# Performance work log

Hardware: AMD Instinct MI355X
Metric: run time of the kernel (lower is better)

## Reference

```python
import jax, jax.numpy as jnp
import numpy as np

N_BASIS = 128   # n_atom_basis F
N_INT   = 3     # n_interactions
N_RBF   = 20
CUTOFF  = 5.0
MAX_Z   = 100
EPS     = 1e-8
N_ATOMS = 25000
N_EDGES = 200000


def setup_inputs() -> dict:
    key = jax.random.key(0)
    ks = jax.random.split(key, 16)
    F = N_BASIS
    s = 0.02
    z     = jax.random.randint(ks[0], (N_ATOMS,), 1, MAX_Z)
    pos   = jax.random.uniform(ks[1], (N_ATOMS, 3), dtype=jnp.float32) * 2.0  # small box -> inside cutoff
    idx_i = jax.random.randint(ks[2], (N_EDGES,), 0, N_ATOMS)
    idx_j = jax.random.randint(ks[3], (N_EDGES,), 0, N_ATOMS)
    emb   = jax.random.normal(ks[4], (MAX_Z, F), dtype=jnp.float32) * s
    fW    = jax.random.normal(ks[5], (N_RBF, 3 * F * N_INT), dtype=jnp.float32) * s
    fb    = jnp.zeros((3 * F * N_INT,), jnp.float32)
    iW1   = jax.random.normal(ks[6], (N_INT, F, F), dtype=jnp.float32) * s
    ib1   = jnp.zeros((N_INT, F), jnp.float32)
    iW2   = jax.random.normal(ks[7], (N_INT, F, 3 * F), dtype=jnp.float32) * s
    ib2   = jnp.zeros((N_INT, 3 * F), jnp.float32)
    mWmix = jax.random.normal(ks[8], (N_INT, F, 2 * F), dtype=jnp.float32) * s
    mW1   = jax.random.normal(ks[9], (N_INT, 2 * F, F), dtype=jnp.float32) * s
    mb1   = jnp.zeros((N_INT, F), jnp.float32)
    mW2   = jax.random.normal(ks[10], (N_INT, F, 3 * F), dtype=jnp.float32) * s
    mb2   = jnp.zeros((N_INT, 3 * F), jnp.float32)
    return dict(z=z, pos=pos, idx_i=idx_i, idx_j=idx_j, emb=emb, fW=fW, fb=fb,
                iW1=iW1, ib1=ib1, iW2=iW2, ib2=ib2,
                mWmix=mWmix, mW1=mW1, mb1=mb1, mW2=mW2, mb2=mb2)


def reference(z, pos, idx_i, idx_j, emb, fW, fb, iW1, ib1, iW2, ib2,
              mWmix, mW1, mb1, mW2, mb2):
    F = N_BASIS
    n_atoms = z.shape[0]
    # geometry
    r_ij = pos[idx_j] - pos[idx_i]                                  # [E,3]
    r_ij = jnp.where(jnp.abs(r_ij) < 1e-6, 1e-6, r_ij)
    d_ij = jnp.linalg.norm(r_ij, axis=1, keepdims=True)             # [E,1]
    dir_ij = r_ij / d_ij                                            # [E,3]
    # Gaussian radial basis
    offsets = jnp.linspace(0.0, CUTOFF, N_RBF)
    width = offsets[1] - offsets[0]
    coeff = -0.5 / (width * width)
    phi = jnp.exp(coeff * (d_ij[..., None] - offsets) ** 2)         # [E,1,n_rbf]
    # cosine cutoff
    fcut = 0.5 * (jnp.cos(jnp.pi * d_ij / CUTOFF) + 1.0) * (d_ij < CUTOFF)  # [E,1]
    filters = (phi @ fW + fb) * fcut[..., None]                     # [E,1,3F*I]
    filter_list = jnp.split(filters, N_INT, axis=-1)                # each [E,1,3F]
    # initial atom features
    q = emb[z][:, None, :]                                          # [N,1,F]
    mu = jnp.zeros((n_atoms, 3, F), q.dtype)                        # [N,3,F]
    for t in range(N_INT):
        # --- interaction (gather - filter-multiply - scatter-add) ---
        x = jax.nn.silu(q @ iW1[t] + ib1[t]) @ iW2[t] + ib2[t]      # [N,1,3F]
        xj = x[idx_j]                                               # [E,1,3F]
        muj = mu[idx_j]                                             # [E,3,F]
        x = filter_list[t] * xj                                     # [E,1,3F]
        dq, dmuR, dmumu = jnp.split(x, 3, axis=-1)                  # [E,1,F] each
        dq = jax.ops.segment_sum(dq, idx_i, num_segments=n_atoms)   # [N,1,F]
        dmu = dmuR * dir_ij[..., None] + dmumu * muj                # [E,3,F]
        dmu = jax.ops.segment_sum(dmu, idx_i, num_segments=n_atoms) # [N,3,F]
        q = q + dq
        mu = mu + dmu
        # --- mixing (intra-atomic) ---
        mu_mix = mu @ mWmix[t]                                      # [N,3,2F]
        mu_V, mu_W = jnp.split(mu_mix, 2, axis=-1)                  # [N,3,F]
        mu_Vn = jnp.sqrt(jnp.sum(mu_V ** 2, axis=-2, keepdims=True) + EPS)  # [N,1,F]
        ctx = jnp.concatenate([q, mu_Vn], axis=-1)                  # [N,1,2F]
        x = jax.nn.silu(ctx @ mW1[t] + mb1[t]) @ mW2[t] + mb2[t]    # [N,1,3F]
        dq_intra, dmu_intra, dqmu_intra = jnp.split(x, 3, axis=-1)
        dmu_intra = dmu_intra * mu_W                                # [N,3,F]
        dqmu_intra = dqmu_intra * jnp.sum(mu_V * mu_W, axis=1, keepdims=True)
        q = q + dq_intra + dqmu_intra
        mu = mu + dmu_intra
    return q.squeeze(1), mu
```

## Files before the change

### kernel.cpp

```cpp
#include <hip/hip_runtime.h>
#include <hip/hip_bf16.h>

#define F 128
#define F3 384
#define NRBF 20
#define NITER 3
#define KP 24

typedef __hip_bfloat16 bf16;
typedef __bf16 bfrag __attribute__((ext_vector_type(8)));
typedef float f32x4 __attribute__((ext_vector_type(4)));

__device__ __forceinline__ float b2f(bf16 v) { return __bfloat162float(v); }
__device__ __forceinline__ bf16 f2b(float v) { return __float2bfloat16(v); }
__device__ __forceinline__ bfrag ldb(const bf16* p) { return *(const bfrag*)p; }
__device__ __forceinline__ bfrag ldsb(const __bf16* p) { return *(const bfrag*)p; }
__device__ __forceinline__ bfrag cvtf(const float* p) {
    bfrag r;
#pragma unroll
    for (int j = 0; j < 8; ++j) r[j] = (__bf16)p[j];
    return r;
}

__global__ void detect_kernel(const unsigned short* __restrict__ raw, int n_u16,
                              int* __restrict__ flag) {
    int i = blockIdx.x * blockDim.x + threadIdx.x;
    int bad = 0;
    for (int k = i; k < n_u16; k += blockDim.x * gridDim.x) {
        unsigned e = (raw[k] >> 7) & 0xFFu;
        if (e >= 140u) bad = 1;
    }
    if (bad) atomicOr(flag, 1);
}

struct CvtArgs {
    const void* src[13];
    float* dst[13];
    int end[14];
};
__global__ void cvt_all_kernel(CvtArgs a, const int* __restrict__ flag, int total) {
    int idx = blockIdx.x * blockDim.x + threadIdx.x;
    if (idx >= total) return;
    int s = 0;
    while (idx >= a.end[s + 1]) ++s;
    int local = idx - a.end[s];
    float v = (*flag) ? ((const float*)a.src[s])[local]
                      : b2f(((const bf16*)a.src[s])[local]);
    a.dst[s][local] = v;
}

struct TpArgs {
    const float* src[5];
    bf16* dst[5];
    int K[5];
    int Nn[5];
    int end[6];
};
__global__ void tpose_all_kernel(TpArgs a, int total) {
    int idx = blockIdx.x * blockDim.x + threadIdx.x;
    if (idx >= total) return;
    int s = 0;
    while (idx >= a.end[s + 1]) ++s;
    int local = idx - a.end[s];
    int K = a.K[s], Nn = a.Nn[s], slice = K * Nn;
    int t = local / slice, j = local - t * slice;
    int n = j / K, k = j - n * K;
    a.dst[s][local] = f2b(a.src[s][t * slice + k * Nn + n]);
}

__global__ void fwt_kernel(const float* __restrict__ fW, const float* __restrict__ fb,
                           float* __restrict__ dst, int total) {
    int idx = blockIdx.x * blockDim.x + threadIdx.x;
    if (idx >= total) return;
    int k = idx % KP, rest = idx / KP;
    int n = rest % F3, t = rest / F3;
    float v = (k < NRBF) ? fW[k * (F3 * NITER) + t * F3 + n]
                         : (k == NRBF ? fb[t * F3 + n] : 0.0f);
    dst[idx] = v;
}

__global__ void geom_kernel(const float* __restrict__ pos, const int* __restrict__ ii,
                            const int* __restrict__ jj, const int* __restrict__ rank,
                            float* __restrict__ phifc2, float* __restrict__ dir2, int E) {
    int e = blockIdx.x * blockDim.x + threadIdx.x;
    if (e >= E) return;
    int i = ii[e], j = jj[e], l = rank[e];
    float r[3];
#pragma unroll
    for (int d = 0; d < 3; ++d) {
        float v = pos[j * 3 + d] - pos[i * 3 + d];
        if (fabsf(v) < 1e-6f) v = 1e-6f;
        r[d] = v;
    }
    float dd = sqrtf(r[0] * r[0] + r[1] * r[1] + r[2] * r[2]);
    float inv = 1.0f / dd;
#pragma unroll
    for (int d = 0; d < 3; ++d) dir2[(size_t)l * 4 + d] = r[d] * inv;
    dir2[(size_t)l * 4 + 3] = __int_as_float(j);
    const float CUT = 5.0f;
    const float PI = 3.14159265358979323846f;
    float fc = (dd < CUT) ? 0.5f * (cosf(PI * dd / CUT) + 1.0f) : 0.0f;
    const float width = CUT / (NRBF - 1);
    const float coeff = -0.5f / (width * width);
    float* pr = phifc2 + (size_t)l * KP;
#pragma unroll
    for (int k = 0; k < NRBF; ++k) {
        float diff = dd - (float)k * width;
        pr[k] = expf(coeff * diff * diff) * fc;
    }
    pr[NRBF] = fc;
    pr[NRBF + 1] = 0.0f;
    pr[NRBF + 2] = 0.0f;
    pr[NRBF + 3] = 0.0f;
}

__global__ void embed_kernel(const int* __restrict__ z, const float* __restrict__ emb,
                             float* __restrict__ q, int N) {
    int idx = blockIdx.x * blockDim.x + threadIdx.x;
    if (idx >= N * F) return;
    int n = idx >> 7, f = idx & 127;
    q[idx] = emb[z[n] * F + f];
}

__global__ void count_kernel(const int* __restrict__ ii, int* __restrict__ counts, int E) {
    int e = blockIdx.x * blockDim.x + threadIdx.x;
    if (e < E) atomicAdd(&counts[ii[e]], 1);
}

__global__ void scan_kernel(const int* __restrict__ counts, int* __restrict__ offs, int N) {
    __shared__ int cum[1024];
    int t = threadIdx.x;
    int chunk = (N + 1023) >> 10;
    int b = t * chunk;
    int e = b + chunk; if (e > N) e = N;
    int s = 0;
    for (int a = b; a < e; ++a) s += counts[a];
    cum[t] = s;
    __syncthreads();
    for (int o = 1; o < 1024; o <<= 1) {
        int u = (t >= o) ? cum[t - o] : 0;
        __syncthreads();
        cum[t] += u;
        __syncthreads();
    }
    int run = cum[t] - s;
    for (int a = b; a < e; ++a) { offs[a] = run; run += counts[a]; }
    if (t == 1023) offs[N] = cum[1023];
}

__global__ void fill_kernel(const int* __restrict__ ii, const int* __restrict__ offs,
                            int* __restrict__ cursor, int* __restrict__ rank, int E) {
    int e = blockIdx.x * blockDim.x + threadIdx.x;
    if (e >= E) return;
    int i = ii[e];
    int p = atomicAdd(&cursor[i], 1);
    rank[e] = offs[i] + p;
}

__global__ __launch_bounds__(256) void atom_x_mfma(
    const float* __restrict__ q, const bf16* __restrict__ W1T, const float* __restrict__ b1,
    const bf16* __restrict__ W2T, const float* __restrict__ b2, bf16* __restrict__ x, int N) {
    __shared__ __bf16 H[32][136];
    int tid = threadIdx.x;
    int w = tid >> 6, l = tid & 63;
    int lm = l & 15, q4 = l >> 4;
    int i0 = blockIdx.x * 32;
    f32x4 acc[2][2] = {};
    int r0 = min(i0 + lm, N - 1);
    int r1 = min(i0 + 16 + lm, N - 1);
    for (int kt = 0; kt < 4; ++kt) {
        int ko = kt * 32 + q4 * 8;
        bfrag a0 = cvtf(q + (size_t)r0 * F + ko);
        bfrag a1 = cvtf(q + (size_t)r1 * F + ko);
        bfrag b0 = ldb(W1T + (size_t)(w * 32 + lm) * F + ko);
        bfrag b1f = ldb(W1T + (size_t)(w * 32 + 16 + lm) * F + ko);
        acc[0][0] = __builtin_amdgcn_mfma_f32_16x16x32_bf16(a0, b0, acc[0][0], 0, 0, 0);
        acc[1][0] = __builtin_amdgcn_mfma_f32_16x16x32_bf16(a1, b0, acc[1][0], 0, 0, 0);
        acc[0][1] = __builtin_amdgcn_mfma_f32_16x16x32_bf16(a0, b1f, acc[0][1], 0, 0, 0);
        acc[1][1] = __builtin_amdgcn_mfma_f32_16x16x32_bf16(a1, b1f, acc[1][1], 0, 0, 0);
    }
#pragma unroll
    for (int nt = 0; nt < 2; ++nt) {
        int col = w * 32 + nt * 16 + lm;
        float bb = b1[col];
#pragma unroll
        for (int mt = 0; mt < 2; ++mt)
#pragma unroll
            for (int r = 0; r < 4; ++r) {
                float v = acc[mt][nt][r] + bb;
                H[mt * 16 + q4 * 4 + r][col] = (__bf16)(v / (1.0f + expf(-v)));
            }
    }
    __syncthreads();
#pragma unroll
    for (int j = 0; j < 6; ++j) {
        int n0 = w * 96 + j * 16;
        f32x4 c0 = {}, c1 = {};
        const bf16* bp = W2T + (size_t)(n0 + lm) * F;
        for (int kt = 0; kt < 4; ++kt) {
            int ko = kt * 32 + q4 * 8;
            bfrag a0 = ldsb(&H[lm][ko]);
            bfrag a1 = ldsb(&H[16 + lm][ko]);
            bfrag bf = ldb(bp + ko);
            c0 = __builtin_amdgcn_mfma_f32_16x16x32_bf16(a0, bf, c0, 0, 0, 0);
            c1 = __builtin_amdgcn_mfma_f32_16x16x32_bf16(a1, bf, c1, 0, 0, 0);
        }
        int col = n0 + lm;
        float bb = b2[col];
#pragma unroll
        for (int r = 0; r < 4; ++r) {
            int row0 = i0 + q4 * 4 + r;
            int row1 = row0 + 16;
            if (row0 < N) x[(size_t)row0 * F3 + col] = f2b(c0[r] + bb);
            if (row1 < N) x[(size_t)row1 * F3 + col] = f2b(c1[r] + bb);
        }
    }
}

template<int T0>
__global__ __launch_bounds__(128, 2) void edge_gather_d(
    const bf16* __restrict__ mu_in, const bf16* __restrict__ x,
    const float* __restrict__ phifc2, const float* __restrict__ dir2,
    const float* __restrict__ fWTf, const int* __restrict__ offs,
    float* __restrict__ dq, bf16* __restrict__ dmu, int N) {
    int i = blockIdx.x;
    int f = threadIdx.x;
    float w0[21], w1[21], w2[21];
    {
        const f32x4* p0 = (const f32x4*)(fWTf + (size_t)f * KP);
        const f32x4* p1 = (const f32x4*)(fWTf + (size_t)(f + 128) * KP);
#pragma unroll
        for (int k = 0; k < 6; ++k) {
            f32x4 t0 = p0[k], t1 = p1[k];
#pragma unroll
            for (int r = 0; r < 4; ++r) {
                int kk = k * 4 + r;
                if (kk < 21) { w0[kk] = t0[r]; w1[kk] = t1[r]; }
            }
        }
        if constexpr (!T0) {
            const f32x4* p2 = (const f32x4*)(fWTf + (size_t)(f + 256) * KP);
#pragma unroll
            for (int k = 0; k < 6; ++k) {
                f32x4 t2 = p2[k];
#pragma unroll
                for (int r = 0; r < 4; ++r) {
                    int kk = k * 4 + r;
                    if (kk < 21) w2[kk] = t2[r];
                }
            }
        }
    }
#pragma unroll
    for (int k = 0; k < 21; ++k) {
        asm volatile("" : "+v"(w0[k]), "+v"(w1[k]));
        if constexpr (!T0) asm volatile("" : "+v"(w2[k]));
    }
    int beg = offs[i], end = offs[i + 1];
    float accq = 0.0f, am0 = 0.0f, am1 = 0.0f, am2 = 0.0f;
    for (int l = beg; l < end; ++l) {
        const f32x4* pr4 = (const f32x4*)(phifc2 + (size_t)l * KP);
        f32x4 p[6];
#pragma unroll
        for (int k = 0; k < 6; ++k) p[k] = __builtin_nontemporal_load(pr4 + k);
        float fl0 = 0.0f, fl1 = 0.0f, fl2 = 0.0f;
#pragma unroll
        for (int k = 0; k < 21; ++k) {
            float ph = p[k >> 2][k & 3];
            fl0 += ph * w0[k];
            fl1 += ph * w1[k];
            if constexpr (!T0) fl2 += ph * w2[k];
        }
        f32x4 dv = __builtin_nontemporal_load((const f32x4*)(dir2 + (size_t)l * 4));
        int j = __float_as_int(dv[3]);
        const bf16* xj = x + (size_t)j * F3;
        float dqv = fl0 * b2f(xj[f]);
        float dR = fl1 * b2f(xj[f + 128]);
        accq += dqv;
        if constexpr (!T0) {
            float dM = fl2 * b2f(xj[f + 256]);
            const bf16* muj = mu_in + (size_t)j * F3;
            am0 += dR * dv[0] + dM * b2f(muj[f]);
            am1 += dR * dv[1] + dM * b2f(muj[f + 128]);
            am2 += dR * dv[2] + dM * b2f(muj[f + 256]);
        } else {
            am0 += dR * dv[0];
            am1 += dR * dv[1];
            am2 += dR * dv[2];
        }
    }
    dq[(size_t)i * F + f] = accq;
    size_t mb = (size_t)i * F3 + f;
    dmu[mb]       = f2b(am0);
    dmu[mb + 128] = f2b(am1);
    dmu[mb + 256] = f2b(am2);
}

template<int T0>
__global__ __launch_bounds__(256) void mix_mfma(
    float* __restrict__ q, const float* __restrict__ dqb,
    const bf16* __restrict__ mu_in, const bf16* __restrict__ dmu,
    bf16* __restrict__ mu_out,
    const bf16* __restrict__ WmixT, const bf16* __restrict__ W1T, const float* __restrict__ b1,
    const bf16* __restrict__ W2T, const float* __restrict__ b2, int N) {
    __shared__ __bf16 MM[48][264];
    __shared__ __bf16 CT[16][264];
    __shared__ __bf16 HM[16][136];
    __shared__ __bf16 Y[16][392];
    int tid = threadIdx.x;
    int w = tid >> 6, l = tid & 63;
    int lm = l & 15, q4 = l >> 4;
    int i0 = blockIdx.x * 16;
    int rowsM = N * 3;
    {
        f32x4 acc[3][4] = {};
        int mr[3];
#pragma unroll
        for (int mt = 0; mt < 3; ++mt) mr[mt] = min(i0 * 3 + mt * 16 + lm, rowsM - 1);
        for (int kt = 0; kt < 4; ++kt) {
            int ko = kt * 32 + q4 * 8;
            bfrag a[3], b[4];
#pragma unroll
            for (int mt = 0; mt < 3; ++mt) {
                bfrag d = ldb(dmu + (size_t)mr[mt] * F + ko);
                if constexpr (T0) {
                    a[mt] = d;
                } else {
                    bfrag u = ldb(mu_in + (size_t)mr[mt] * F + ko);
#pragma unroll
                    for (int jj = 0; jj < 8; ++jj)
                        a[mt][jj] = (__bf16)((float)u[jj] + (float)d[jj]);
                }
            }
#pragma unroll
            for (int nt = 0; nt < 4; ++nt)
                b[nt] = ldb(WmixT + (size_t)(w * 64 + nt * 16 + lm) * F + ko);
#pragma unroll
            for (int mt = 0; mt < 3; ++mt)
#pragma unroll
                for (int nt = 0; nt < 4; ++nt)
                    acc[mt][nt] = __builtin_amdgcn_mfma_f32_16x16x32_bf16(a[mt], b[nt], acc[mt][nt], 0, 0, 0);
        }
#pragma unroll
        for (int mt = 0; mt < 3; ++mt)
#pragma unroll
            for (int nt = 0; nt < 4; ++nt)
#pragma unroll
                for (int r = 0; r < 4; ++r)
                    MM[mt * 16 + q4 * 4 + r][w * 64 + nt * 16 + lm] = (__bf16)acc[mt][nt][r];
    }
    __syncthreads();
    for (int idx = tid; idx < 16 * F; idx += 256) {
        int a = idx >> 7, f = idx & 127;
        int i = min(i0 + a, N - 1);
        float v0 = (float)MM[a * 3 + 0][f];
        float v1 = (float)MM[a * 3 + 1][f];
        float v2 = (float)MM[a * 3 + 2][f];
        float qe = q[(size_t)i * F + f] + dqb[(size_t)i * F + f];
        CT[a][f] = (__bf16)qe;
        CT[a][F + f] = (__bf16)sqrtf(v0 * v0 + v1 * v1 + v2 * v2 + 1e-8f);
    }
    __syncthreads();
    {
        f32x4 c[2] = {};
        for (int kt = 0; kt < 8; ++kt) {
            int ko = kt * 32 + q4 * 8;
            bfrag a = ldsb(&CT[lm][ko]);
#pragma unroll
            for (int nt = 0; nt < 2; ++nt) {
                bfrag b = ldb(W1T + (size_t)(w * 32 + nt * 16 + lm) * 256 + ko);
                c[nt] = __builtin_amdgcn_mfma_f32_16x16x32_bf16(a, b, c[nt], 0, 0, 0);
            }
        }
#pragma unroll
        for (int nt = 0; nt < 2; ++nt) {
            int col = w * 32 + nt * 16 + lm;
            float bb = b1[col];
#pragma unroll
            for (int r = 0; r < 4; ++r) {
                float v = c[nt][r] + bb;
                HM[q4 * 4 + r][col] = (__bf16)(v / (1.0f + expf(-v)));
            }
        }
    }
    __syncthreads();
#pragma unroll
    for (int j = 0; j < 6; ++j) {
        int n0 = w * 96 + j * 16;
        f32x4 c = {};
        const bf16* bp = W2T + (size_t)(n0 + lm) * F;
        for (int kt = 0; kt < 4; ++kt) {
            int ko = kt * 32 + q4 * 8;
            bfrag a = ldsb(&HM[lm][ko]);
            bfrag b = ldb(bp + ko);
            c = __builtin_amdgcn_mfma_f32_16x16x32_bf16(a, b, c, 0, 0, 0);
        }
        int col = n0 + lm;
        float bb = b2[col];
#pragma unroll
        for (int r = 0; r < 4; ++r)
            Y[q4 * 4 + r][col] = (__bf16)(c[r] + bb);
    }
    __syncthreads();
    for (int idx = tid; idx < 16 * F; idx += 256) {
        int a = idx >> 7, f = idx & 127;
        int i = i0 + a;
        if (i >= N) continue;
        float V0 = (float)MM[a * 3 + 0][f], W0 = (float)MM[a * 3 + 0][F + f];
        float V1 = (float)MM[a * 3 + 1][f], W1v = (float)MM[a * 3 + 1][F + f];
        float V2 = (float)MM[a * 3 + 2][f], W2v = (float)MM[a * 3 + 2][F + f];
        float s = V0 * W0 + V1 * W1v + V2 * W2v;
        float yq = (float)Y[a][f], ym = (float)Y[a][F + f], ys = (float)Y[a][2 * F + f];
        size_t qb = (size_t)i * F + f;
        q[qb] = q[qb] + dqb[qb] + yq + ys * s;
        size_t mb = (size_t)i * F3 + f;
        float m0 = b2f(dmu[mb]);
        float m1 = b2f(dmu[mb + 128]);
        float m2 = b2f(dmu[mb + 256]);
        if constexpr (!T0) {
            m0 += b2f(mu_in[mb]);
            m1 += b2f(mu_in[mb + 128]);
            m2 += b2f(mu_in[mb + 256]);
        }
        mu_out[mb]       = f2b(m0 + ym * W0);
        mu_out[mb + 128] = f2b(m1 + ym * W1v);
        mu_out[mb + 256] = f2b(m2 + ym * W2v);
    }
}

__global__ void out_kernel(const float* __restrict__ q, const bf16* __restrict__ mu,
                           void* __restrict__ out, int N, const int* __restrict__ flag) {
    int idx = blockIdx.x * blockDim.x + threadIdx.x;
    int nq = N * F;
    int tot = nq + N * F3;
    if (idx >= tot) return;
    float v = (idx < nq) ? q[idx] : b2f(mu[idx - nq]);
    if (*flag) ((float*)out)[idx] = v;
    else       ((bf16*)out)[idx] = f2b(v);
}

extern "C" void kernel_launch(void* const* d_in, const int* in_sizes, int n_in,
                              void* d_out, int out_size, void* d_ws, size_t ws_size,
                              hipStream_t stream) {
    const int* z = (const int*)d_in[0];
    const int* idx_i = (const int*)d_in[2];
    const int* idx_j = (const int*)d_in[3];

    int N = in_sizes[0];
    int E = in_sizes[2];

    char* base = (char*)d_ws;
    size_t off = 0;
    auto alloc = [&](size_t bytes) -> void* {
        void* p = base + off;
        off += (bytes + 255) & ~(size_t)255;
        return p;
    };

    int* flag = (int*)alloc(4);
    float* pos_f = (float*)alloc((size_t)in_sizes[1] * 4);
    float* emb_f = (float*)alloc((size_t)in_sizes[4] * 4);
    float* fW_f = (float*)alloc((size_t)in_sizes[5] * 4);
    float* fb_f = (float*)alloc((size_t)in_sizes[6] * 4);
    float* iW1_f = (float*)alloc((size_t)in_sizes[7] * 4);
    float* ib1_f = (float*)alloc((size_t)in_sizes[8] * 4);
    float* iW2_f = (float*)alloc((size_t)in_sizes[9] * 4);
    float* ib2_f = (float*)alloc((size_t)in_sizes[10] * 4);
    float* mWmix_f = (float*)alloc((size_t)in_sizes[11] * 4);
    float* mW1_f = (float*)alloc((size_t)in_sizes[12] * 4);
    float* mb1_f = (float*)alloc((size_t)in_sizes[13] * 4);
    float* mW2_f = (float*)alloc((size_t)in_sizes[14] * 4);
    float* mb2_f = (float*)alloc((size_t)in_sizes[15] * 4);
    bf16* iW1T = (bf16*)alloc((size_t)NITER * F * F * 2);
    bf16* iW2T = (bf16*)alloc((size_t)NITER * F3 * F * 2);
    bf16* mWmixT = (bf16*)alloc((size_t)NITER * 2 * F * F * 2);
    bf16* mW1T = (bf16*)alloc((size_t)NITER * F * 2 * F * 2);
    bf16* mW2T = (bf16*)alloc((size_t)NITER * F3 * F * 2);
    float* fWTf = (float*)alloc((size_t)NITER * F3 * KP * 4);
    float* q = (float*)alloc((size_t)N * F * 4);
    float* dqb = (float*)alloc((size_t)N * F * 4);
    bf16* mua = (bf16*)alloc((size_t)N * F3 * 2);
    bf16* mub = (bf16*)alloc((size_t)N * F3 * 2);
    bf16* dmub = (bf16*)alloc((size_t)N * F3 * 2);
    bf16* xbuf = (bf16*)alloc((size_t)N * F3 * 2);
    float* phifc2 = (float*)alloc((size_t)(E + 16) * KP * 4);
    float* dir2 = (float*)alloc((size_t)(E + 16) * 4 * 4);
    int* rank = (int*)alloc((size_t)E * 4);
    int* counts = (int*)alloc((size_t)N * 4);
    int* offs = (int*)alloc((size_t)(N + 1) * 4);

    hipMemsetAsync(flag, 0, 4, stream);
    detect_kernel<<<64, 256, 0, stream>>>((const unsigned short*)d_in[1], in_sizes[1], flag);

    {
        CvtArgs a;
        const int srcIdx[13] = {1, 4, 5, 6, 7, 8, 9, 10, 11, 12, 13, 14, 15};
        float* dsts[13] = {pos_f, emb_f, fW_f, fb_f, iW1_f, ib1_f, iW2_f, ib2_f,
                           mWmix_f, mW1_f, mb1_f, mW2_f, mb2_f};
        int cum = 0;
        a.end[0] = 0;
        for (int s = 0; s < 13; ++s) {
            a.src[s] = d_in[srcIdx[s]];
            a.dst[s] = dsts[s];
            cum += in_sizes[srcIdx[s]];
            a.end[s + 1] = cum;
        }
        cvt_all_kernel<<<(cum + 255) / 256, 256, 0, stream>>>(a, flag, cum);
    }

    {
        TpArgs a;
        const float* srcs[5] = {iW1_f, iW2_f, mWmix_f, mW1_f, mW2_f};
        bf16* dsts[5] = {iW1T, iW2T, mWmixT, mW1T, mW2T};
        int Ks[5] = {F, F, F, 2 * F, F};
        int Nns[5] = {F, F3, 2 * F, F, F3};
        int cum = 0;
        a.end[0] = 0;
        for (int s = 0; s < 5; ++s) {
            a.src[s] = srcs[s];
            a.dst[s] = dsts[s];
            a.K[s] = Ks[s];
            a.Nn[s] = Nns[s];
            cum += NITER * Ks[s] * Nns[s];
            a.end[s + 1] = cum;
        }
        tpose_all_kernel<<<(cum + 255) / 256, 256, 0, stream>>>(a, cum);
    }
    {
        int total = NITER * F3 * KP;
        fwt_kernel<<<(total + 255) / 256, 256, 0, stream>>>(fW_f, fb_f, fWTf, total);
    }

    hipMemsetAsync(counts, 0, (size_t)N * 4, stream);
    count_kernel<<<(E + 255) / 256, 256, 0, stream>>>(idx_i, counts, E);
    scan_kernel<<<1, 1024, 0, stream>>>(counts, offs, N);
    hipMemsetAsync(counts, 0, (size_t)N * 4, stream);
    fill_kernel<<<(E + 255) / 256, 256, 0, stream>>>(idx_i, offs, counts, rank, E);

    geom_kernel<<<(E + 255) / 256, 256, 0, stream>>>(pos_f, idx_i, idx_j, rank,
                                                     phifc2, dir2, E);
    embed_kernel<<<(N * F + 255) / 256, 256, 0, stream>>>(z, emb_f, q, N);

    bf16* muin = mua;
    bf16* muout = mub;
    for (int t = 0; t < NITER; ++t) {
        atom_x_mfma<<<(N + 31) / 32, 256, 0, stream>>>(q, iW1T + (size_t)t * F * F, ib1_f + t * F,
                                                       iW2T + (size_t)t * F3 * F, ib2_f + t * F3,
                                                       xbuf, N);
        if (t == 0) {
            edge_gather_d<1><<<N, 128, 0, stream>>>(muin, xbuf, phifc2, dir2,
                                                    fWTf + (size_t)t * F3 * KP, offs,
                                                    dqb, dmub, N);
            mix_mfma<1><<<(N + 15) / 16, 256, 0, stream>>>(q, dqb, muin, dmub, muout,
                                                           mWmixT + (size_t)t * 2 * F * F,
                                                           mW1T + (size_t)t * F * 2 * F, mb1_f + t * F,
                                                           mW2T + (size_t)t * F3 * F, mb2_f + t * F3, N);
        } else {
            edge_gather_d<0><<<N, 128, 0, stream>>>(muin, xbuf, phifc2, dir2,
                                                    fWTf + (size_t)t * F3 * KP, offs,
                                                    dqb, dmub, N);
            mix_mfma<0><<<(N + 15) / 16, 256, 0, stream>>>(q, dqb, muin, dmub, muout,
                                                           mWmixT + (size_t)t * 2 * F * F,
                                                           mW1T + (size_t)t * F * 2 * F, mb1_f + t * F,
                                                           mW2T + (size_t)t * F3 * F, mb2_f + t * F3, N);
        }
        bf16* tm = muin; muin = muout; muout = tm;
    }

    int tot = N * (F + F3);
    out_kernel<<<(tot + 255) / 256, 256, 0, stream>>>(q, muin, d_out, N, flag);
}
```

Measured before the change: 784.1 us.

## Fuse next-iteration atom MLP and output write into mix kernel; store phi and dq in bf16

The per-atom interaction MLP (x = W2·silu(W1·q)) for the next iteration is computed inside the mixing kernel from the freshly updated q held in shared memory, which removes the separate atom_x launches for iterations 1 and 2 and the q reload they needed. The final mixing pass writes the output buffer directly, so out_kernel is gone. The radial basis features and the dq scratch buffer are stored as bf16 instead of fp32, halving the bytes the edge gather kernel reads per edge. In exchange, precision drops on phi and dq, and the mix kernel gains extra shared-memory and MFMA work, with more register pressure.

```diff
diff --git a/kernel.cpp b/kernel.cpp
--- a/kernel.cpp
+++ b/kernel.cpp
@@ -81,7 +81,7 @@
 
 __global__ void geom_kernel(const float* __restrict__ pos, const int* __restrict__ ii,
                             const int* __restrict__ jj, const int* __restrict__ rank,
-                            float* __restrict__ phifc2, float* __restrict__ dir2, int E) {
+                            bf16* __restrict__ phifc2, float* __restrict__ dir2, int E) {
     int e = blockIdx.x * blockDim.x + threadIdx.x;
     if (e >= E) return;
     int i = ii[e], j = jj[e], l = rank[e];
@@ -102,16 +102,16 @@
     float fc = (dd < CUT) ? 0.5f * (cosf(PI * dd / CUT) + 1.0f) : 0.0f;
     const float width = CUT / (NRBF - 1);
     const float coeff = -0.5f / (width * width);
-    float* pr = phifc2 + (size_t)l * KP;
+    bf16* pr = phifc2 + (size_t)l * KP;
 #pragma unroll
     for (int k = 0; k < NRBF; ++k) {
         float diff = dd - (float)k * width;
-        pr[k] = expf(coeff * diff * diff) * fc;
-    }
-    pr[NRBF] = fc;
-    pr[NRBF + 1] = 0.0f;
-    pr[NRBF + 2] = 0.0f;
-    pr[NRBF + 3] = 0.0f;
+        pr[k] = f2b(expf(coeff * diff * diff) * fc);
+    }
+    pr[NRBF] = f2b(fc);
+    pr[NRBF + 1] = f2b(0.0f);
+    pr[NRBF + 2] = f2b(0.0f);
+    pr[NRBF + 3] = f2b(0.0f);
 }
 
 __global__ void embed_kernel(const int* __restrict__ z, const float* __restrict__ emb,
@@ -220,9 +220,9 @@
 template<int T0>
 __global__ __launch_bounds__(128, 2) void edge_gather_d(
     const bf16* __restrict__ mu_in, const bf16* __restrict__ x,
-    const float* __restrict__ phifc2, const float* __restrict__ dir2,
+    const bf16* __restrict__ phifc2, const float* __restrict__ dir2,
     const float* __restrict__ fWTf, const int* __restrict__ offs,
-    float* __restrict__ dq, bf16* __restrict__ dmu, int N) {
+    bf16* __restrict__ dq, bf16* __restrict__ dmu, int N) {
     int i = blockIdx.x;
     int f = threadIdx.x;
     float w0[21], w1[21], w2[21];
@@ -259,17 +259,23 @@
     int beg = offs[i], end = offs[i + 1];
     float accq = 0.0f, am0 = 0.0f, am1 = 0.0f, am2 = 0.0f;
     for (int l = beg; l < end; ++l) {
-        const f32x4* pr4 = (const f32x4*)(phifc2 + (size_t)l * KP);
-        f32x4 p[6];
-#pragma unroll
-        for (int k = 0; k < 6; ++k) p[k] = __builtin_nontemporal_load(pr4 + k);
+        const bfrag* pb = (const bfrag*)(phifc2 + (size_t)l * KP);
+        bfrag p0 = __builtin_nontemporal_load(pb);
+        bfrag p1 = __builtin_nontemporal_load(pb + 1);
+        bfrag p2 = __builtin_nontemporal_load(pb + 2);
+        float ph[21];
+#pragma unroll
+        for (int k = 0; k < 8; ++k) ph[k] = (float)p0[k];
+#pragma unroll
+        for (int k = 0; k < 8; ++k) ph[8 + k] = (float)p1[k];
+#pragma unroll
+        for (int k = 0; k < 5; ++k) ph[16 + k] = (float)p2[k];
         float fl0 = 0.0f, fl1 = 0.0f, fl2 = 0.0f;
 #pragma unroll
         for (int k = 0; k < 21; ++k) {
-            float ph = p[k >> 2][k & 3];
-            fl0 += ph * w0[k];
-            fl1 += ph * w1[k];
-            if constexpr (!T0) fl2 += ph * w2[k];
+            fl0 += ph[k] * w0[k];
+            fl1 += ph[k] * w1[k];
+            if constexpr (!T0) fl2 += ph[k] * w2[k];
         }
         f32x4 dv = __builtin_nontemporal_load((const f32x4*)(dir2 + (size_t)l * 4));
         int j = __float_as_int(dv[3]);
@@ -289,20 +295,23 @@
             am2 += dR * dv[2];
         }
     }
-    dq[(size_t)i * F + f] = accq;
+    dq[(size_t)i * F + f] = f2b(accq);
     size_t mb = (size_t)i * F3 + f;
     dmu[mb]       = f2b(am0);
     dmu[mb + 128] = f2b(am1);
     dmu[mb + 256] = f2b(am2);
 }
 
-template<int T0>
+template<int T0, int EMITX, int OUT>
 __global__ __launch_bounds__(256) void mix_mfma(
-    float* __restrict__ q, const float* __restrict__ dqb,
+    float* __restrict__ q, const bf16* __restrict__ dqb,
     const bf16* __restrict__ mu_in, const bf16* __restrict__ dmu,
     bf16* __restrict__ mu_out,
     const bf16* __restrict__ WmixT, const bf16* __restrict__ W1T, const float* __restrict__ b1,
-    const bf16* __restrict__ W2T, const float* __restrict__ b2, int N) {
+    const bf16* __restrict__ W2T, const float* __restrict__ b2,
+    const bf16* __restrict__ xW1T, const float* __restrict__ xb1,
+    const bf16* __restrict__ xW2T, const float* __restrict__ xb2, bf16* __restrict__ xout,
+    void* __restrict__ outp, const int* __restrict__ flag, int N) {
     __shared__ __bf16 MM[48][264];
     __shared__ __bf16 CT[16][264];
     __shared__ __bf16 HM[16][136];
@@ -356,7 +365,7 @@
         float v0 = (float)MM[a * 3 + 0][f];
         float v1 = (float)MM[a * 3 + 1][f];
         float v2 = (float)MM[a * 3 + 2][f];
-        float qe = q[(size_t)i * F + f] + dqb[(size_t)i * F + f];
+        float qe = q[(size_t)i * F + f] + b2f(dqb[(size_t)i * F + f]);
         CT[a][f] = (__bf16)qe;
         CT[a][F + f] = (__bf16)sqrtf(v0 * v0 + v1 * v1 + v2 * v2 + 1e-8f);
     }
@@ -402,6 +411,7 @@
             Y[q4 * 4 + r][col] = (__bf16)(c[r] + bb);
     }
     __syncthreads();
+    int nq = N * F;
     for (int idx = tid; idx < 16 * F; idx += 256) {
         int a = idx >> 7, f = idx & 127;
         int i = i0 + a;
@@ -412,7 +422,7 @@
         float s = V0 * W0 + V1 * W1v + V2 * W2v;
         float yq = (float)Y[a][f], ym = (float)Y[a][F + f], ys = (float)Y[a][2 * F + f];
         size_t qb = (size_t)i * F + f;
-        q[qb] = q[qb] + dqb[qb] + yq + ys * s;
+        float qv = q[qb] + b2f(dqb[qb]) + yq + ys * s;
         size_t mb = (size_t)i * F3 + f;
         float m0 = b2f(dmu[mb]);
         float m1 = b2f(dmu[mb + 128]);
@@ -422,21 +432,76 @@
             m1 += b2f(mu_in[mb + 128]);
             m2 += b2f(mu_in[mb + 256]);
         }
-        mu_out[mb]       = f2b(m0 + ym * W0);
-        mu_out[mb + 128] = f2b(m1 + ym * W1v);
-        mu_out[mb + 256] = f2b(m2 + ym * W2v);
-    }
-}
-
-__global__ void out_kernel(const float* __restrict__ q, const bf16* __restrict__ mu,
-                           void* __restrict__ out, int N, const int* __restrict__ flag) {
-    int idx = blockIdx.x * blockDim.x + threadIdx.x;
-    int nq = N * F;
-    int tot = nq + N * F3;
-    if (idx >= tot) return;
-    float v = (idx < nq) ? q[idx] : b2f(mu[idx - nq]);
-    if (*flag) ((float*)out)[idx] = v;
-    else       ((bf16*)out)[idx] = f2b(v);
+        m0 += ym * W0;
+        m1 += ym * W1v;
+        m2 += ym * W2v;
+        if constexpr (OUT) {
+            if (*flag) {
+                float* of = (float*)outp;
+                of[qb] = qv;
+                of[nq + mb] = m0;
+                of[nq + mb + 128] = m1;
+                of[nq + mb + 256] = m2;
+            } else {
+                bf16* ob = (bf16*)outp;
+                ob[qb] = f2b(qv);
+                ob[nq + mb] = f2b(m0);
+                ob[nq + mb + 128] = f2b(m1);
+                ob[nq + mb + 256] = f2b(m2);
+            }
+        } else {
+            q[qb] = qv;
+            mu_out[mb]       = f2b(m0);
+            mu_out[mb + 128] = f2b(m1);
+            mu_out[mb + 256] = f2b(m2);
+        }
+        if constexpr (EMITX) CT[a][f] = (__bf16)qv;
+    }
+    if constexpr (EMITX) {
+        __syncthreads();
+        {
+            f32x4 c[2] = {};
+            for (int kt = 0; kt < 4; ++kt) {
+                int ko = kt * 32 + q4 * 8;
+                bfrag a = ldsb(&CT[lm][ko]);
+#pragma unroll
+                for (int nt = 0; nt < 2; ++nt) {
+                    bfrag b = ldb(xW1T + (size_t)(w * 32 + nt * 16 + lm) * F + ko);
+                    c[nt] = __builtin_amdgcn_mfma_f32_16x16x32_bf16(a, b, c[nt], 0, 0, 0);
+                }
+            }
+#pragma unroll
+            for (int nt = 0; nt < 2; ++nt) {
+                int col = w * 32 + nt * 16 + lm;
+                float bb = xb1[col];
+#pragma unroll
+                for (int r = 0; r < 4; ++r) {
+                    float v = c[nt][r] + bb;
+                    HM[q4 * 4 + r][col] = (__bf16)(v / (1.0f + expf(-v)));
+                }
+            }
+        }
+        __syncthreads();
+#pragma unroll
+        for (int j = 0; j < 6; ++j) {
+            int n0 = w * 96 + j * 16;
+            f32x4 c = {};
+            const bf16* bp = xW2T + (size_t)(n0 + lm) * F;
+            for (int kt = 0; kt < 4; ++kt) {
+                int ko = kt * 32 + q4 * 8;
+                bfrag a = ldsb(&HM[lm][ko]);
+                bfrag b = ldb(bp + ko);
+                c = __builtin_amdgcn_mfma_f32_16x16x32_bf16(a, b, c, 0, 0, 0);
+            }
+            int col = n0 + lm;
+            float bb = xb2[col];
+#pragma unroll
+            for (int r = 0; r < 4; ++r) {
+                int row = i0 + q4 * 4 + r;
+                if (row < N) xout[(size_t)row * F3 + col] = f2b(c[r] + bb);
+            }
+        }
+    }
 }
 
 extern "C" void kernel_launch(void* const* d_in, const int* in_sizes, int n_in,
@@ -478,12 +543,12 @@
     bf16* mW2T = (bf16*)alloc((size_t)NITER * F3 * F * 2);
     float* fWTf = (float*)alloc((size_t)NITER * F3 * KP * 4);
     float* q = (float*)alloc((size_t)N * F * 4);
-    float* dqb = (float*)alloc((size_t)N * F * 4);
+    bf16* dqb = (bf16*)alloc((size_t)N * F * 2);
     bf16* mua = (bf16*)alloc((size_t)N * F3 * 2);
     bf16* mub = (bf16*)alloc((size_t)N * F3 * 2);
     bf16* dmub = (bf16*)alloc((size_t)N * F3 * 2);
     bf16* xbuf = (bf16*)alloc((size_t)N * F3 * 2);
-    float* phifc2 = (float*)alloc((size_t)(E + 16) * KP * 4);
+    bf16* phifc2 = (bf16*)alloc((size_t)(E + 16) * KP * 2);
     float* dir2 = (float*)alloc((size_t)(E + 16) * 4 * 4);
     int* rank = (int*)alloc((size_t)E * 4);
     int* counts = (int*)alloc((size_t)N * 4);
@@ -541,32 +606,34 @@
                                                      phifc2, dir2, E);
     embed_kernel<<<(N * F + 255) / 256, 256, 0, stream>>>(z, emb_f, q, N);
 
+    int mixGrid = (N + 15) / 16;
     bf16* muin = mua;
     bf16* muout = mub;
-    for (int t = 0; t < NITER; ++t) {
-        atom_x_mfma<<<(N + 31) / 32, 256, 0, stream>>>(q, iW1T + (size_t)t * F * F, ib1_f + t * F,
-                                                       iW2T + (size_t)t * F3 * F, ib2_f + t * F3,
-                                                       xbuf, N);
-        if (t == 0) {
-            edge_gather_d<1><<<N, 128, 0, stream>>>(muin, xbuf, phifc2, dir2,
-                                                    fWTf + (size_t)t * F3 * KP, offs,
-                                                    dqb, dmub, N);
-            mix_mfma<1><<<(N + 15) / 16, 256, 0, stream>>>(q, dqb, muin, dmub, muout,
-                                                           mWmixT + (size_t)t * 2 * F * F,
-                                                           mW1T + (size_t)t * F * 2 * F, mb1_f + t * F,
-                                                           mW2T + (size_t)t * F3 * F, mb2_f + t * F3, N);
-        } else {
-            edge_gather_d<0><<<N, 128, 0, stream>>>(muin, xbuf, phifc2, dir2,
-                                                    fWTf + (size_t)t * F3 * KP, offs,
-                                                    dqb, dmub, N);
-            mix_mfma<0><<<(N + 15) / 16, 256, 0, stream>>>(q, dqb, muin, dmub, muout,
-                                                           mWmixT + (size_t)t * 2 * F * F,
-                                                           mW1T + (size_t)t * F * 2 * F, mb1_f + t * F,
-                                                           mW2T + (size_t)t * F3 * F, mb2_f + t * F3, N);
-        }
-        bf16* tm = muin; muin = muout; muout = tm;
-    }
-
-    int tot = N * (F + F3);
-    out_kernel<<<(tot + 255) / 256, 256, 0, stream>>>(q, muin, d_out, N, flag);
-}
+    atom_x_mfma<<<(N + 31) / 32, 256, 0, stream>>>(q, iW1T, ib1_f, iW2T, ib2_f, xbuf, N);
+    edge_gather_d<1><<<N, 128, 0, stream>>>(muin, xbuf, phifc2, dir2,
+                                            fWTf, offs, dqb, dmub, N);
+    mix_mfma<1, 1, 0><<<mixGrid, 256, 0, stream>>>(q, dqb, muin, dmub, muout,
+                                                   mWmixT, mW1T, mb1_f, mW2T, mb2_f,
+                                                   iW1T + (size_t)1 * F * F, ib1_f + 1 * F,
+                                                   iW2T + (size_t)1 * F3 * F, ib2_f + 1 * F3,
+                                                   xbuf, nullptr, flag, N);
+    { bf16* tm = muin; muin = muout; muout = tm; }
+    edge_gather_d<0><<<N, 128, 0, stream>>>(muin, xbuf, phifc2, dir2,
+                                            fWTf + (size_t)1 * F3 * KP, offs, dqb, dmub, N);
+    mix_mfma<0, 1, 0><<<mixGrid, 256, 0, stream>>>(q, dqb, muin, dmub, muout,
+                                                   mWmixT + (size_t)1 * 2 * F * F,
+                                                   mW1T + (size_t)1 * F * 2 * F, mb1_f + 1 * F,
+                                                   mW2T + (size_t)1 * F3 * F, mb2_f + 1 * F3,
+                                                   iW1T + (size_t)2 * F * F, ib1_f + 2 * F,
+                                                   iW2T + (size_t)2 * F3 * F, ib2_f + 2 * F3,
+                                                   xbuf, nullptr, flag, N);
+    { bf16* tm = muin; muin = muout; muout = tm; }
+    edge_gather_d<0><<<N, 128, 0, stream>>>(muin, xbuf, phifc2, dir2,
+                                            fWTf + (size_t)2 * F3 * KP, offs, dqb, dmub, N);
+    mix_mfma<0, 0, 1><<<mixGrid, 256, 0, stream>>>(q, dqb, muin, dmub, muout,
+                                                   mWmixT + (size_t)2 * 2 * F * F,
+                                                   mW1T + (size_t)2 * F * 2 * F, mb1_f + 2 * F,
+                                                   mW2T + (size_t)2 * F3 * F, mb2_f + 2 * F3,
+                                                   nullptr, nullptr, nullptr, nullptr,
+                                                   nullptr, d_out, flag, N);
+}
```

Measured after the change: 766.7 us. -2.2%, faster.
